# Optimization experiments

Measured on AMD Instinct MI355X. Metric: run time of the kernel, lower is better.

## Reference

```python
import jax, jax.numpy as jnp
import numpy as np

B, T = 64, 512
N_EMB, HIDDEN, VOCAB = 768, 256, 3072


def setup_inputs() -> dict:
    key = jax.random.key(0)
    ks = jax.random.split(key, 5)
    def xavier(k, shape):
        bound = float(np.sqrt(6.0 / (shape[0] + shape[1])))
        return jax.random.uniform(k, shape, jnp.float32, -bound, bound)
    return {
        "idx": jax.random.randint(ks[0], (B, T), 0, VOCAB),
        "emb_table": jax.random.normal(ks[1], (VOCAB, N_EMB), jnp.float32),
        "Wxh": xavier(ks[2], (N_EMB, HIDDEN)),
        "Whh": xavier(ks[3], (HIDDEN, HIDDEN)),
        "Wy": xavier(ks[4], (HIDDEN, VOCAB)),
        "By": jnp.zeros((VOCAB,), jnp.float32),
        "Bh": jnp.zeros((HIDDEN,), jnp.float32),
    }


def reference(idx, emb_table, Wxh, Whh, Wy, By, Bh):
    # embedded: [B, T, E] -> scan over time with hidden carry [B, H]
    embedded = emb_table[idx]                      # gather
    xWxh = jnp.einsum('bte,eh->tbh', embedded, Wxh)  # precompute input projection

    def step(hidden, x_t):
        hidden = jnp.tanh(x_t + hidden @ Whh + Bh)
        return hidden, None

    h0 = jnp.zeros((idx.shape[0], Whh.shape[0]), embedded.dtype)
    hidden, _ = jax.lax.scan(step, h0, xWxh)
    # return_sequences=False: only the last step's output is returned
    out = hidden @ Wy + By
    return out, hidden
```

## Files before the change

kernel.cpp:

```cpp
#include <hip/hip_runtime.h>
#include <hip/hip_bf16.h>

typedef _Float16 half8 __attribute__((ext_vector_type(8)));
typedef float f32x4 __attribute__((ext_vector_type(4)));

#define B_SZ 64
#define T_SZ 512
#define E_SZ 768
#define H_SZ 256
#define V_SZ 3072

#define WS_P     0u
#define WS_WT    16777216u
#define WS_WF    17170432u
#define WS_H     17301504u

static __device__ __forceinline__ float fast_tanh(float x) {
  float e = __builtin_amdgcn_exp2f(x * 2.8853900817779268f);
  return 1.0f - 2.0f * __builtin_amdgcn_rcpf(1.0f + e);
}

__global__ __launch_bounds__(256) void k0_convert(
    const float* __restrict__ Wxh,
    const float* __restrict__ Whh,
    _Float16* __restrict__ Wtf,
    _Float16* __restrict__ Wf)
{
  int gid = blockIdx.x * 256 + threadIdx.x;
  if (gid < 24 * 8192) {
    int j = gid & 7, f = (gid >> 3) & 1023, ki = gid >> 13;
    int kb = (f >> 4) & 3;
    int n_ = ((f >> 6) << 4) | (f & 15);
    int e  = ki * 32 + kb * 8 + j;
    Wtf[gid] = (_Float16)Wxh[e * H_SZ + n_];
  }
  if (gid < 65536) {
    int j = gid & 7, lane = (gid >> 3) & 63, kt = (gid >> 9) & 7, nt = gid >> 12;
    int quad = lane >> 4, n16 = lane & 15;
    int row = kt * 32 + quad * 8 + j, col = nt * 16 + n16;
    Wf[gid] = (_Float16)Whh[row * H_SZ + col];
  }
}

__global__ __launch_bounds__(256) void k1_xproj(
    const float* __restrict__ emb,
    const _Float16* __restrict__ Wtf,
    _Float16* __restrict__ P)
{
  const int tid  = threadIdx.x;
  const int w    = tid >> 6;
  const int lane = tid & 63;
  const int m16  = lane & 15;
  const int quad = lane >> 4;
  const int r = blockIdx.x * 64 + w * 16 + m16;
  const float* Arow = emb + (size_t)r * E_SZ + quad * 8;

  __shared__ __align__(16) _Float16 bp[2][16 * 64 * 8];
  uint4 stg[4];
#pragma unroll
  for (int pp = 0; pp < 4; ++pp)
    stg[pp] = *(const uint4*)(Wtf + (size_t)(tid + 256 * pp) * 8);
  f32x4 af0 = *(const f32x4*)(Arow);
  f32x4 af1 = *(const f32x4*)(Arow + 4);

  f32x4 acc[16];
#pragma unroll
  for (int n = 0; n < 16; ++n) { f32x4 z = {0.f, 0.f, 0.f, 0.f}; acc[n] = z; }

#pragma unroll
  for (int pp = 0; pp < 4; ++pp)
    *(uint4*)(bp[0] + (size_t)(tid + 256 * pp) * 8) = stg[pp];
  __syncthreads();

#pragma unroll 1
  for (int ki = 0; ki < 24; ++ki) {
    const _Float16* cur = bp[ki & 1];
    f32x4 af0n = af0, af1n = af1;
    if (ki < 23) {
#pragma unroll
      for (int pp = 0; pp < 4; ++pp)
        stg[pp] = *(const uint4*)(Wtf + (size_t)(ki + 1) * 8192
                                      + (size_t)(tid + 256 * pp) * 8);
      af0n = *(const f32x4*)(Arow + (ki + 1) * 32);
      af1n = *(const f32x4*)(Arow + (ki + 1) * 32 + 4);
    }
    half8 a;
#pragma unroll
    for (int e = 0; e < 4; ++e) { a[e] = (_Float16)af0[e]; a[4 + e] = (_Float16)af1[e]; }
#pragma unroll
    for (int nt = 0; nt < 16; ++nt) {
      half8 bb = *(const half8*)(cur + (size_t)(nt * 64 + lane) * 8);
      acc[nt] = __builtin_amdgcn_mfma_f32_16x16x32_f16(a, bb, acc[nt], 0, 0, 0);
    }
    if (ki < 23) {
#pragma unroll
      for (int pp = 0; pp < 4; ++pp)
        *(uint4*)(bp[(ki + 1) & 1] + (size_t)(tid + 256 * pp) * 8) = stg[pp];
      __syncthreads();
    }
    af0 = af0n; af1 = af1n;
  }
  const int rbase = blockIdx.x * 64 + w * 16 + quad * 4;
#pragma unroll
  for (int nt = 0; nt < 16; ++nt) {
    const int col = nt * 16 + m16;
#pragma unroll
    for (int rg = 0; rg < 4; ++rg) {
      P[(size_t)(rbase + rg) * H_SZ + col] = (_Float16)acc[nt][rg];
    }
  }
}

#define LDFRAG(C, KT, R0, R1, R2, R3) { \
  uint4 q = Wf4[(((size_t)(w * 4 + C) * 8 + KT) * 64) + lane]; \
  asm volatile("v_accvgpr_write_b32 a" #R0 ", %0" :: "v"(q.x) : "a" #R0); \
  asm volatile("v_accvgpr_write_b32 a" #R1 ", %0" :: "v"(q.y) : "a" #R1); \
  asm volatile("v_accvgpr_write_b32 a" #R2 ", %0" :: "v"(q.z) : "a" #R2); \
  asm volatile("v_accvgpr_write_b32 a" #R3 ", %0" :: "v"(q.w) : "a" #R3); }

#define MFMA_K0(A0, Z) \
  asm volatile( \
    "v_mfma_f32_16x16x32_f16 %[t0], %[a], a[0:3],   %[z]\n\t" \
    "v_mfma_f32_16x16x32_f16 %[t1], %[a], a[32:35], %[z]\n\t" \
    "v_mfma_f32_16x16x32_f16 %[t2], %[a], a[64:67], %[z]\n\t" \
    "v_mfma_f32_16x16x32_f16 %[t3], %[a], a[96:99], %[z]" \
    : [t0] "=&v"(acc0), [t1] "=&v"(acc1), [t2] "=&v"(acc2), [t3] "=&v"(acc3) \
    : [a] "v"(A0), [z] "v"(Z));

#define MFMA_KT(A0, B0, B1, B2, B3) \
  asm volatile( \
    "v_mfma_f32_16x16x32_f16 %[t0], %[a], a[" #B0 "], %[t0]\n\t" \
    "v_mfma_f32_16x16x32_f16 %[t1], %[a], a[" #B1 "], %[t1]\n\t" \
    "v_mfma_f32_16x16x32_f16 %[t2], %[a], a[" #B2 "], %[t2]\n\t" \
    "v_mfma_f32_16x16x32_f16 %[t3], %[a], a[" #B3 "], %[t3]" \
    : [t0] "+v"(acc0), [t1] "+v"(acc1), [t2] "+v"(acc2), [t3] "+v"(acc3) \
    : [a] "v"(A0));

#define MFMA_K7(A0, B0, B1, B2, B3) \
  asm volatile( \
    "v_mfma_f32_16x16x32_f16 %[t0], %[a], a[" #B0 "], %[t0]\n\t" \
    "v_mfma_f32_16x16x32_f16 %[t1], %[a], a[" #B1 "], %[t1]\n\t" \
    "v_mfma_f32_16x16x32_f16 %[t2], %[a], a[" #B2 "], %[t2]\n\t" \
    "v_mfma_f32_16x16x32_f16 %[t3], %[a], a[" #B3 "], %[t3]\n\t" \
    "s_nop 7\n\t" \
    "s_nop 7" \
    : [t0] "+v"(acc0), [t1] "+v"(acc1), [t2] "+v"(acc2), [t3] "+v"(acc3) \
    : [a] "v"(A0));

__global__ __launch_bounds__(256) void k2_rnn(
    const _Float16* __restrict__ Wf,
    const _Float16* __restrict__ P,
    const int* __restrict__ idx,
    const float* __restrict__ Bh,
    float* __restrict__ hout,
    float* __restrict__ hidout)
{
  const int b    = blockIdx.x;
  const int tid  = threadIdx.x;
  const int w    = tid >> 6;
  const int lane = tid & 63;
  const int quad = lane >> 4;
  __shared__ __align__(16) _Float16 hb[2][H_SZ];
  const uint4* Wf4 = (const uint4*)Wf;

  LDFRAG(0,0,  0,  1,  2,  3)  LDFRAG(0,1,  4,  5,  6,  7)
  LDFRAG(0,2,  8,  9, 10, 11)  LDFRAG(0,3, 12, 13, 14, 15)
  LDFRAG(0,4, 16, 17, 18, 19)  LDFRAG(0,5, 20, 21, 22, 23)
  LDFRAG(0,6, 24, 25, 26, 27)  LDFRAG(0,7, 28, 29, 30, 31)
  LDFRAG(1,0, 32, 33, 34, 35)  LDFRAG(1,1, 36, 37, 38, 39)
  LDFRAG(1,2, 40, 41, 42, 43)  LDFRAG(1,3, 44, 45, 46, 47)
  LDFRAG(1,4, 48, 49, 50, 51)  LDFRAG(1,5, 52, 53, 54, 55)
  LDFRAG(1,6, 56, 57, 58, 59)  LDFRAG(1,7, 60, 61, 62, 63)
  LDFRAG(2,0, 64, 65, 66, 67)  LDFRAG(2,1, 68, 69, 70, 71)
  LDFRAG(2,2, 72, 73, 74, 75)  LDFRAG(2,3, 76, 77, 78, 79)
  LDFRAG(2,4, 80, 81, 82, 83)  LDFRAG(2,5, 84, 85, 86, 87)
  LDFRAG(2,6, 88, 89, 90, 91)  LDFRAG(2,7, 92, 93, 94, 95)
  LDFRAG(3,0, 96, 97, 98, 99)  LDFRAG(3,1,100,101,102,103)
  LDFRAG(3,2,104,105,106,107)  LDFRAG(3,3,108,109,110,111)
  LDFRAG(3,4,112,113,114,115)  LDFRAG(3,5,116,117,118,119)
  LDFRAG(3,6,120,121,122,123)  LDFRAG(3,7,124,125,126,127)

  const float bhj = Bh[tid];
  const int* idxb = idx + b * T_SZ;
  int rowN = idxb[1];
  _Float16 xq = P[(size_t)idxb[0] * H_SZ + tid];
  f32x4 zero4 = {0.f, 0.f, 0.f, 0.f};
  asm volatile("" : "+v"(zero4));
  hb[1][tid] = (_Float16)0.f;
  float hval = 0.f;
  __syncthreads();

#pragma unroll 1
  for (int t = 0; t < T_SZ; ++t) {
    int t2 = t + 2; t2 = t2 > 511 ? 511 : t2;
    int rowN2 = idxb[t2];
    _Float16 xn = P[(size_t)rowN * H_SZ + tid];
    const _Float16* hr = hb[(t + 1) & 1];
    half8 va0 = *(const half8*)(hr +   0 + quad * 8);
    half8 va1 = *(const half8*)(hr +  32 + quad * 8);
    half8 va2 = *(const half8*)(hr +  64 + quad * 8);
    half8 va3 = *(const half8*)(hr +  96 + quad * 8);
    half8 va4 = *(const half8*)(hr + 128 + quad * 8);
    half8 va5 = *(const half8*)(hr + 160 + quad * 8);
    half8 va6 = *(const half8*)(hr + 192 + quad * 8);
    half8 va7 = *(const half8*)(hr + 224 + quad * 8);
    f32x4 acc0, acc1, acc2, acc3;
    MFMA_K0(va0, zero4)
    MFMA_KT(va1,   4:7,  36:39,  68:71, 100:103)
    MFMA_KT(va2,  8:11,  40:43,  72:75, 104:107)
    MFMA_KT(va3, 12:15,  44:47,  76:79, 108:111)
    MFMA_KT(va4, 16:19,  48:51,  80:83, 112:115)
    MFMA_KT(va5, 20:23,  52:55,  84:87, 116:119)
    MFMA_KT(va6, 24:27,  56:59,  88:91, 120:123)
    MFMA_K7(va7, 28:31,  60:63,  92:95, 124:127)
    float v0 = acc0[0], v1 = acc1[0], v2 = acc2[0], v3 = acc3[0];
    float ylo = (quad & 1) ? v1 : v0;
    float yhi = (quad & 1) ? v3 : v2;
    float y   = (quad & 2) ? yhi : ylo;
    hval = fast_tanh(y + (float)xq + bhj);
    hb[t & 1][tid] = (_Float16)hval;
    __syncthreads();
    xq = xn; rowN = rowN2;
  }
  hout[b * H_SZ + tid] = hval;
  hidout[b * H_SZ + tid] = hval;
}

__global__ __launch_bounds__(256) void k3_out(
    const float* __restrict__ h,
    const float* __restrict__ Wy,
    const float* __restrict__ By,
    float* __restrict__ out)
{
  __shared__ float hs[H_SZ];
  const int c = blockIdx.x;
  const int b = blockIdx.y;
  const int v = c * 256 + threadIdx.x;
  hs[threadIdx.x] = h[b * H_SZ + threadIdx.x];
  __syncthreads();
  float acc = By[v];
#pragma unroll 8
  for (int jj = 0; jj < H_SZ; ++jj) {
    acc += hs[jj] * Wy[(size_t)jj * V_SZ + v];
  }
  out[(size_t)b * V_SZ + v] = acc;
}

extern "C" void kernel_launch(void* const* d_in, const int* in_sizes, int n_in,
                              void* d_out, int out_size, void* d_ws, size_t ws_size,
                              hipStream_t stream)
{
  const int*   idx = (const int*)d_in[0];
  const float* emb = (const float*)d_in[1];
  const float* Wxh = (const float*)d_in[2];
  const float* Whh = (const float*)d_in[3];
  const float* Wy  = (const float*)d_in[4];
  const float* By  = (const float*)d_in[5];
  const float* Bh  = (const float*)d_in[6];

  char* ws = (char*)d_ws;
  _Float16* P    = (_Float16*)(ws + WS_P);
  _Float16* Wtf  = (_Float16*)(ws + WS_WT);
  _Float16* Wf   = (_Float16*)(ws + WS_WF);
  float*    hbuf = (float*)(ws + WS_H);

  float* out    = (float*)d_out;
  float* hidout = out + (size_t)B_SZ * V_SZ;

  k0_convert<<<768, 256, 0, stream>>>(Wxh, Whh, Wtf, Wf);
  k1_xproj  <<<48, 256, 0, stream>>>(emb, Wtf, P);
  k2_rnn    <<<64, 256, 0, stream>>>(Wf, P, idx, Bh, hbuf, hidout);
  k3_out    <<<dim3(12, 64), 256, 0, stream>>>(hbuf, Wy, By, out);
}
```

Measured before the change: 370.0 us.

## Unroll recurrence by two with deeper prefetch; coalesce weight conversion; split output accumulators

The recurrent loop is unrolled by two with fixed ping-pong buffers, and the gathered input-projection values are prefetched two steps ahead instead of one. This removes the per-step buffer-index arithmetic and hides more of the gather latency on the serial critical path. The weight-conversion kernel now reads fp32 sources in coalesced order and scatters the fp16 writes. The output GEMV uses four independent accumulators to shorten its FMA dependency chain. The cost is some extra register pressure in the recurrence kernel, and the summation order changes slightly in the output.

```diff
diff --git a/kernel.cpp b/kernel.cpp
--- a/kernel.cpp
+++ b/kernel.cpp
@@ -27,18 +27,20 @@
     _Float16* __restrict__ Wf)
 {
   int gid = blockIdx.x * 256 + threadIdx.x;
-  if (gid < 24 * 8192) {
-    int j = gid & 7, f = (gid >> 3) & 1023, ki = gid >> 13;
-    int kb = (f >> 4) & 3;
-    int n_ = ((f >> 6) << 4) | (f & 15);
-    int e  = ki * 32 + kb * 8 + j;
-    Wtf[gid] = (_Float16)Wxh[e * H_SZ + n_];
+  if (gid < E_SZ * H_SZ) {
+    int e = gid >> 8, n = gid & 255;
+    float v = Wxh[gid];
+    int ki = e >> 5, kb = (e >> 3) & 3, j = e & 7;
+    int f  = ((n >> 4) << 6) | (kb << 4) | (n & 15);
+    Wtf[(size_t)ki * 8192 + (size_t)f * 8 + j] = (_Float16)v;
   }
   if (gid < 65536) {
-    int j = gid & 7, lane = (gid >> 3) & 63, kt = (gid >> 9) & 7, nt = gid >> 12;
-    int quad = lane >> 4, n16 = lane & 15;
-    int row = kt * 32 + quad * 8 + j, col = nt * 16 + n16;
-    Wf[gid] = (_Float16)Whh[row * H_SZ + col];
+    int row = gid >> 8, col = gid & 255;
+    float v = Whh[gid];
+    int kt = row >> 5, quad = (row >> 3) & 3, j = row & 7;
+    int nt = col >> 4;
+    int lane = (quad << 4) | (col & 15);
+    Wf[(((size_t)(nt * 8 + kt) * 64 + lane) * 8) + j] = (_Float16)v;
   }
 }
 
@@ -182,46 +184,59 @@
 
   const float bhj = Bh[tid];
   const int* idxb = idx + b * T_SZ;
-  int rowN = idxb[1];
-  _Float16 xq = P[(size_t)idxb[0] * H_SZ + tid];
+  int rowA = idxb[2];
+  int rowB = idxb[3];
+  _Float16 xA = P[(size_t)idxb[0] * H_SZ + tid];
+  _Float16 xB = P[(size_t)idxb[1] * H_SZ + tid];
   f32x4 zero4 = {0.f, 0.f, 0.f, 0.f};
   asm volatile("" : "+v"(zero4));
   hb[1][tid] = (_Float16)0.f;
   float hval = 0.f;
   __syncthreads();
 
+#define K2_STEP(HR, HW, XV)                                              \
+  {                                                                      \
+    const _Float16* hr = (HR);                                           \
+    half8 va0 = *(const half8*)(hr +   0 + quad * 8);                    \
+    half8 va1 = *(const half8*)(hr +  32 + quad * 8);                    \
+    half8 va2 = *(const half8*)(hr +  64 + quad * 8);                    \
+    half8 va3 = *(const half8*)(hr +  96 + quad * 8);                    \
+    half8 va4 = *(const half8*)(hr + 128 + quad * 8);                    \
+    half8 va5 = *(const half8*)(hr + 160 + quad * 8);                    \
+    half8 va6 = *(const half8*)(hr + 192 + quad * 8);                    \
+    half8 va7 = *(const half8*)(hr + 224 + quad * 8);                    \
+    f32x4 acc0, acc1, acc2, acc3;                                        \
+    MFMA_K0(va0, zero4)                                                  \
+    MFMA_KT(va1,   4:7,  36:39,  68:71, 100:103)                         \
+    MFMA_KT(va2,  8:11,  40:43,  72:75, 104:107)                         \
+    MFMA_KT(va3, 12:15,  44:47,  76:79, 108:111)                         \
+    MFMA_KT(va4, 16:19,  48:51,  80:83, 112:115)                         \
+    MFMA_KT(va5, 20:23,  52:55,  84:87, 116:119)                         \
+    MFMA_KT(va6, 24:27,  56:59,  88:91, 120:123)                         \
+    MFMA_K7(va7, 28:31,  60:63,  92:95, 124:127)                         \
+    float v0 = acc0[0], v1 = acc1[0], v2 = acc2[0], v3 = acc3[0];        \
+    float ylo = (quad & 1) ? v1 : v0;                                    \
+    float yhi = (quad & 1) ? v3 : v2;                                    \
+    float y   = (quad & 2) ? yhi : ylo;          \
+    hval = fast_tanh(y + (XV) + bhj);                                    \
+    (HW)[tid] = (_Float16)hval;                                          \
+    __syncthreads();                                                     \
+  }
+
 #pragma unroll 1
-  for (int t = 0; t < T_SZ; ++t) {
-    int t2 = t + 2; t2 = t2 > 511 ? 511 : t2;
-    int rowN2 = idxb[t2];
-    _Float16 xn = P[(size_t)rowN * H_SZ + tid];
-    const _Float16* hr = hb[(t + 1) & 1];
-    half8 va0 = *(const half8*)(hr +   0 + quad * 8);
-    half8 va1 = *(const half8*)(hr +  32 + quad * 8);
-    half8 va2 = *(const half8*)(hr +  64 + quad * 8);
-    half8 va3 = *(const half8*)(hr +  96 + quad * 8);
-    half8 va4 = *(const half8*)(hr + 128 + quad * 8);
-    half8 va5 = *(const half8*)(hr + 160 + quad * 8);
-    half8 va6 = *(const half8*)(hr + 192 + quad * 8);
-    half8 va7 = *(const half8*)(hr + 224 + quad * 8);
-    f32x4 acc0, acc1, acc2, acc3;
-    MFMA_K0(va0, zero4)
-    MFMA_KT(va1,   4:7,  36:39,  68:71, 100:103)
-    MFMA_KT(va2,  8:11,  40:43,  72:75, 104:107)
-    MFMA_KT(va3, 12:15,  44:47,  76:79, 108:111)
-    MFMA_KT(va4, 16:19,  48:51,  80:83, 112:115)
-    MFMA_KT(va5, 20:23,  52:55,  84:87, 116:119)
-    MFMA_KT(va6, 24:27,  56:59,  88:91, 120:123)
-    MFMA_K7(va7, 28:31,  60:63,  92:95, 124:127)
-    float v0 = acc0[0], v1 = acc1[0], v2 = acc2[0], v3 = acc3[0];
-    float ylo = (quad & 1) ? v1 : v0;
-    float yhi = (quad & 1) ? v3 : v2;
-    float y   = (quad & 2) ? yhi : ylo;
-    hval = fast_tanh(y + (float)xq + bhj);
-    hb[t & 1][tid] = (_Float16)hval;
-    __syncthreads();
-    xq = xn; rowN = rowN2;
-  }
+  for (int tt = 0; tt < 256; ++tt) {
+    float xvA = (float)xA;
+    xA = P[(size_t)rowA * H_SZ + tid];
+    int t4 = 2 * tt + 4; t4 = t4 > 511 ? 511 : t4;
+    rowA = idxb[t4];
+    K2_STEP(hb[1], hb[0], xvA)
+    float xvB = (float)xB;
+    xB = P[(size_t)rowB * H_SZ + tid];
+    int t5 = 2 * tt + 5; t5 = t5 > 511 ? 511 : t5;
+    rowB = idxb[t5];
+    K2_STEP(hb[0], hb[1], xvB)
+  }
+#undef K2_STEP
   hout[b * H_SZ + tid] = hval;
   hidout[b * H_SZ + tid] = hval;
 }
@@ -238,12 +253,15 @@
   const int v = c * 256 + threadIdx.x;
   hs[threadIdx.x] = h[b * H_SZ + threadIdx.x];
   __syncthreads();
-  float acc = By[v];
-#pragma unroll 8
-  for (int jj = 0; jj < H_SZ; ++jj) {
-    acc += hs[jj] * Wy[(size_t)jj * V_SZ + v];
-  }
-  out[(size_t)b * V_SZ + v] = acc;
+  float a0 = By[v], a1 = 0.f, a2 = 0.f, a3 = 0.f;
+#pragma unroll 4
+  for (int jj = 0; jj < H_SZ; jj += 4) {
+    a0 += hs[jj + 0] * Wy[(size_t)(jj + 0) * V_SZ + v];
+    a1 += hs[jj + 1] * Wy[(size_t)(jj + 1) * V_SZ + v];
+    a2 += hs[jj + 2] * Wy[(size_t)(jj + 2) * V_SZ + v];
+    a3 += hs[jj + 3] * Wy[(size_t)(jj + 3) * V_SZ + v];
+  }
+  out[(size_t)b * V_SZ + v] = (a0 + a1) + (a2 + a3);
 }
 
 extern "C" void kernel_launch(void* const* d_in, const int* in_sizes, int n_in,
```

Result: faster. 357.6 us, median of 2 (-3.4%).
